# Optimization experiments

Measured on AMD Instinct MI355X. Metric: run time of the kernel, lower is better.

Reference implementation:

```python
import jax, jax.numpy as jnp
import numpy as np
import math

B, L, D, MAXL = 4, 4096, 1024, 16384


def setup_inputs() -> dict:
    key = jax.random.key(0)
    ks = jax.random.split(key, 12)
    s = 0.02
    def w(k, shape):
        return jax.random.normal(k, shape, jnp.float32) * s
    return {
        "x": jax.random.normal(ks[0], (B, L, D), jnp.float32),
        "pos_phases": jax.random.normal(ks[1], (MAXL, D), jnp.float32) * math.pi,
        "Wpv": w(ks[2], (D, D)), "bpv": jnp.zeros((D,), jnp.float32),
        "Wk": w(ks[3], (D, D)), "bk": jnp.zeros((D,), jnp.float32),
        "Wkv": w(ks[4], (D, D)), "bkv": jnp.zeros((D,), jnp.float32),
        "Wg1": w(ks[5], (2 * D, D)), "bg1": jnp.zeros((D,), jnp.float32),
        "Wg2": w(ks[6], (D, 1)), "bg2": jnp.zeros((1,), jnp.float32),
        "Wb1": w(ks[7], (D, D // 2)), "bb1": jnp.zeros((D // 2,), jnp.float32),
        "Wb2": w(ks[8], (D // 2, 2)), "bb2": jnp.zeros((2,), jnp.float32),
        "ln_g": jnp.ones((D,), jnp.float32), "ln_b": jnp.zeros((D,), jnp.float32),
        "Wo": w(ks[9], (D, D)), "bo": jnp.zeros((D,), jnp.float32),
    }


def _shift1(a):
    # torch.roll(a, 1, dims=1) with a[:, 0] = 0
    return jnp.concatenate([jnp.zeros_like(a[:, :1]), a[:, :-1]], axis=1)


def reference(x, pos_phases, Wpv, bpv, Wk, bk, Wkv, bkv, Wg1, bg1, Wg2, bg2,
              Wb1, bb1, Wb2, bb2, ln_g, ln_b, Wo, bo):
    Bq, Lq, Dq = x.shape
    sqrtD = jnp.sqrt(jnp.float32(Dq))

    # positional phasor memory
    pp = pos_phases[:Lq]                      # [L, D]
    pos_cos, pos_sin = jnp.cos(pp), jnp.sin(pp)
    pos_values = x @ Wpv + bpv                # [B, L, D]
    pos_mem_cos = jnp.cumsum(pos_cos * pos_values, axis=1)
    pos_mem_sin = jnp.cumsum(pos_sin * pos_values, axis=1)
    pos_ret = (pos_cos * pos_mem_cos + pos_sin * pos_mem_sin) / sqrtD

    # key-value phasor memory
    key_ph = jnp.tanh(x @ Wk + bk) * jnp.pi
    key_cos, key_sin = jnp.cos(key_ph), jnp.sin(key_ph)
    kv_values = x @ Wkv + bkv

    x_shifted = _shift1(x)
    gate_in = jnp.concatenate([x, x_shifted], axis=-1)       # [B, L, 2D]
    gh = jax.nn.gelu(gate_in @ Wg1 + bg1, approximate=False)
    value_gates = jax.nn.sigmoid(gh @ Wg2 + bg2)             # [B, L, 1]

    kc_s = _shift1(key_cos)
    ks_s = _shift1(key_sin)
    kv_mem_cos = jnp.cumsum(kc_s * kv_values * value_gates, axis=1)
    kv_mem_sin = jnp.cumsum(ks_s * kv_values * value_gates, axis=1)
    gate_cumsum = jnp.maximum(jnp.cumsum(value_gates, axis=1), 1.0)
    kv_ret = (key_cos * kv_mem_cos + key_sin * kv_mem_sin) / (jnp.sqrt(gate_cumsum) * sqrtD)

    # blend
    bh = jax.nn.gelu(x @ Wb1 + bb1, approximate=False)
    bw = jax.nn.softmax(bh @ Wb2 + bb2, axis=-1)             # [B, L, 2]
    blended = bw[..., 0:1] * pos_ret + bw[..., 1:2] * kv_ret

    # to_out: LayerNorm then Linear
    mu = jnp.mean(blended, axis=-1, keepdims=True)
    var = jnp.var(blended, axis=-1, keepdims=True)
    ln = (blended - mu) / jnp.sqrt(var + 1e-5) * ln_g + ln_b
    return x + ln @ Wo + bo
```

## Files before the change

### kernel.cpp

```cpp
#include <hip/hip_runtime.h>
#include <hip/hip_bf16.h>
#include <math.h>

using bf16 = __hip_bfloat16;
typedef __bf16 v8bf __attribute__((ext_vector_type(8)));
typedef float v4f __attribute__((ext_vector_type(4)));

#define B_ 4
#define L_ 4096
#define D_ 1024
#define M_ (B_*L_)
#define CCH 128
#define LCH (L_/CCH)
#define NF 3584

__device__ __forceinline__ float bf2f(bf16 v){ return __bfloat162float(v); }
__device__ __forceinline__ bf16 f2bf(float v){ return __float2bfloat16(v); }
__device__ __forceinline__ float us2f(ushort u){ union{unsigned u32; float f;}c; c.u32=((unsigned)u)<<16; return c.f; }
__device__ __forceinline__ ushort f2us(float v){ bf16 h=__float2bfloat16(v); return *(ushort*)&h; }
__device__ __forceinline__ float h2f(ushort u){ union{ushort s; _Float16 h;}c; c.s=u; return (float)c.h; }
__device__ __forceinline__ ushort f2h(float v){ union{ushort s; _Float16 h;}c; c.h=(_Float16)v; return c.s; }

__device__ __forceinline__ void g2l16(const void* g, void* l){
  __builtin_amdgcn_global_load_lds(
    (const __attribute__((address_space(1))) unsigned int*)g,
    (__attribute__((address_space(3))) unsigned int*)l, 16, 0, 0);
}

__global__ void k_zeroN(float* __restrict__ p, int n){
  int i = blockIdx.x*256 + threadIdx.x;
  if (i < n) p[i] = 0.0f;
}

__global__ void k_cvt(const float* __restrict__ in, bf16* __restrict__ out){
  int i = (blockIdx.x*256 + threadIdx.x)*4;
  float4 v = *(const float4*)(in + i);
  out[i]   = f2bf(v.x);
  out[i+1] = f2bf(v.y);
  out[i+2] = f2bf(v.z);
  out[i+3] = f2bf(v.w);
}

__global__ void k_cvt_pp(const float* __restrict__ in, ushort* __restrict__ out){
  int i = (blockIdx.x*256 + threadIdx.x)*4;
  float4 v = *(const float4*)(in + i);
  out[i]   = f2h(v.x);
  out[i+1] = f2h(v.y);
  out[i+2] = f2h(v.z);
  out[i+3] = f2h(v.w);
}

__global__ void k_ctr(const float* __restrict__ in, bf16* __restrict__ out, int R, int C){
  __shared__ float tile[32][33];
  int c0 = blockIdx.x*32, r0 = blockIdx.y*32;
  #pragma unroll
  for (int i=0;i<32;i+=8)
    tile[threadIdx.y+i][threadIdx.x] = in[(size_t)(r0+threadIdx.y+i)*C + c0+threadIdx.x];
  __syncthreads();
  #pragma unroll
  for (int i=0;i<32;i+=8)
    out[(size_t)(c0+threadIdx.y+i)*R + r0+threadIdx.x] = f2bf(tile[threadIdx.x][threadIdx.y+i]);
}

__global__ void k_pack_bias(const float* __restrict__ bpv, const float* __restrict__ bk,
                            const float* __restrict__ bkv, const float* __restrict__ bb1,
                            float* __restrict__ bf){
  int i = blockIdx.x*256 + threadIdx.x;
  float v;
  if (i < 1024) v = bpv[i];
  else if (i < 2048) v = bk[i-1024];
  else if (i < 3072) v = bkv[i-2048];
  else v = bb1[i-3072];
  bf[i] = v;
}

__device__ __forceinline__ float geluf(float v){
  return 0.5f*v*(1.0f + erff(v*0.70710678118654752f));
}
__device__ __forceinline__ float fast_tanh(float v){
  float a = fabsf(v);
  float e = __expf(-2.0f*a);
  float t = (1.0f - e)/(1.0f + e);
  return copysignf(t, v);
}

#define BM 256
#define BN 256
#define BK 64

template<int EPI, bool CONCAT>
__global__ __launch_bounds__(512) void k_gemm(
    const bf16* __restrict__ A, int lda,
    const bf16* __restrict__ Bt, int ldb,
    const float* __restrict__ bias,
    const bf16* __restrict__ zeros,
    bf16* __restrict__ o_pv, ushort* __restrict__ o_kp, bf16* __restrict__ o_kv,
    const float* __restrict__ Wv2, const float* __restrict__ Wb2f,
    float* __restrict__ gaccp, float* __restrict__ bwaccp,
    float* __restrict__ outf, const float* __restrict__ residf,
    int N, int Ktot)
{
  __shared__ __align__(16) ushort As[2*BM*BK];
  __shared__ __align__(16) ushort Bs[2*BN*BK];
  int tid = threadIdx.x;
  int lane = tid & 63, wave = tid >> 6;
  int wm = wave >> 2, wn = wave & 3;
  int bn = blockIdx.x * BN, bm = blockIdx.y * BM;

  v4f zero = {0.f,0.f,0.f,0.f};
  v4f acc[8][4];
  #pragma unroll
  for (int i=0;i<8;i++)
    #pragma unroll
    for (int j=0;j<4;j++) acc[i][j] = zero;

  int mr = lane & 15, g4 = lane >> 4;
  int srow = lane >> 3, sseg = lane & 7;

  auto stage = [&](int t, int buf){
    int kk = t*BK;
    ushort* Ad = As + buf*(BM*BK);
    ushort* Bd = Bs + buf*(BN*BK);
    #pragma unroll
    for (int p=0;p<4;p++){
      int r = p*64 + wave*8 + srow;
      const bf16* src;
      if (!CONCAT || kk < D_) {
        src = A + (size_t)(bm + r)*lda + (size_t)kk + sseg*8;
      } else {
        int m = bm + r;
        int l = m & (L_-1);
        src = (l==0) ? (zeros + sseg*8)
                     : (A + (size_t)(m-1)*lda + (size_t)(kk - D_) + sseg*8);
      }
      g2l16(src, Ad + (size_t)(p*64 + wave*8)*BK);
    }
    #pragma unroll
    for (int p=0;p<4;p++){
      int r = p*64 + wave*8 + srow;
      g2l16(Bt + (size_t)(bn + r)*ldb + (size_t)kk + sseg*8,
            Bd + (size_t)(p*64 + wave*8)*BK);
    }
  };

  auto compute = [&](int buf){
    const ushort* Ab = As + buf*(BM*BK);
    const ushort* Bb = Bs + buf*(BN*BK);
    #pragma unroll
    for (int ks=0; ks<2; ks++){
      v8bf a[8], b[4];
      #pragma unroll
      for (int i=0;i<8;i++) a[i] = *(const v8bf*)&Ab[(wm*128 + i*16 + mr)*BK + ks*32 + g4*8];
      #pragma unroll
      for (int j=0;j<4;j++) b[j] = *(const v8bf*)&Bb[(wn*64  + j*16 + mr)*BK + ks*32 + g4*8];
      #pragma unroll
      for (int i=0;i<8;i++)
        #pragma unroll
        for (int j=0;j<4;j++)
          acc[i][j] = __builtin_amdgcn_mfma_f32_16x16x32_bf16(a[i], b[j], acc[i][j], 0, 0, 0);
    }
  };

  int nt = Ktot / BK;
  stage(0, 0);
  for (int t=0; t<nt; ++t){
    if (t+1 < nt){
      stage(t+1, (t+1)&1);
      asm volatile("s_waitcnt vmcnt(8)" ::: "memory");
    } else {
      asm volatile("s_waitcnt vmcnt(0)" ::: "memory");
    }
    asm volatile("s_barrier" ::: "memory");
    compute(t&1);
    asm volatile("s_waitcnt lgkmcnt(0)" ::: "memory");
    asm volatile("s_barrier" ::: "memory");
  }

  int lr = lane >> 4, lc = lane & 15;
  if (EPI == 3){
    #pragma unroll
    for (int i=0;i<8;i++){
      #pragma unroll
      for (int j=0;j<4;j++){
        int col  = bn + wn*64 + j*16 + lc;
        int row0 = bm + wm*128 + i*16 + lr*4;
        float bias_v = bias[col];
        #pragma unroll
        for (int rr=0; rr<4; rr++){
          size_t idx = (size_t)(row0+rr)*N + col;
          outf[idx] = acc[i][j][rr] + bias_v + residf[idx];
        }
      }
    }
  } else if (EPI == 2){
    #pragma unroll
    for (int i=0;i<8;i++){
      float red[4] = {0.f,0.f,0.f,0.f};
      #pragma unroll
      for (int j=0;j<4;j++){
        int col = bn + wn*64 + j*16 + lc;
        float bias_v = bias[col];
        float wv = Wv2[col];
        #pragma unroll
        for (int rr=0; rr<4; rr++){
          float v = acc[i][j][rr] + bias_v;
          red[rr] += geluf(v) * wv;
        }
      }
      int row0 = bm + wm*128 + i*16 + lr*4;
      #pragma unroll
      for (int rr=0; rr<4; rr++){
        float r = red[rr];
        r += __shfl_xor(r,1); r += __shfl_xor(r,2);
        r += __shfl_xor(r,4); r += __shfl_xor(r,8);
        if (lc == 0) atomicAdd(&gaccp[row0+rr], r);
      }
    }
  } else {
    if (bn < 3072){
      #pragma unroll
      for (int i=0;i<8;i++){
        #pragma unroll
        for (int j=0;j<4;j++){
          int col  = bn + wn*64 + j*16 + lc;
          int row0 = bm + wm*128 + i*16 + lr*4;
          float bias_v = bias[col];
          #pragma unroll
          for (int rr=0; rr<4; rr++){
            int row = row0 + rr;
            float v = acc[i][j][rr] + bias_v;
            if (bn < 1024) {
              o_pv[(size_t)row*1024 + col] = f2bf(v);
            } else if (bn < 2048) {
              float kp = fast_tanh(v) * 3.14159265358979323846f;
              o_kp[(size_t)row*1024 + (col-1024)] = f2h(kp);
            } else {
              o_kv[(size_t)row*1024 + (col-2048)] = f2bf(v);
            }
          }
        }
      }
    } else {
      #pragma unroll
      for (int i=0;i<8;i++){
        float r0[4] = {0.f,0.f,0.f,0.f};
        float r1[4] = {0.f,0.f,0.f,0.f};
        #pragma unroll
        for (int j=0;j<4;j++){
          int col = bn + wn*64 + j*16 + lc;
          float bias_v = bias[col];
          int kb = col - 3072;
          float w0 = Wb2f[kb*2], w1 = Wb2f[kb*2+1];
          #pragma unroll
          for (int rr=0; rr<4; rr++){
            float v = acc[i][j][rr] + bias_v;
            float gl = geluf(v);
            r0[rr] += gl*w0;
            r1[rr] += gl*w1;
          }
        }
        int row0 = bm + wm*128 + i*16 + lr*4;
        #pragma unroll
        for (int rr=0; rr<4; rr++){
          float a = r0[rr], b = r1[rr];
          a += __shfl_xor(a,1); a += __shfl_xor(a,2); a += __shfl_xor(a,4); a += __shfl_xor(a,8);
          b += __shfl_xor(b,1); b += __shfl_xor(b,2); b += __shfl_xor(b,4); b += __shfl_xor(b,8);
          if (lc == 0){
            atomicAdd(&bwaccp[(size_t)(row0+rr)*2],   a);
            atomicAdd(&bwaccp[(size_t)(row0+rr)*2+1], b);
          }
        }
      }
    }
  }
}

__global__ __launch_bounds__(1024) void k_gscan(const float* __restrict__ gacc,
                                                const float* __restrict__ bg2,
                                                float* __restrict__ g, float* __restrict__ gc){
  __shared__ float sa[1024];
  int b = blockIdx.x, tid = threadIdx.x;
  int base = b*L_ + tid*4;
  float bb = bg2[0];
  float v0 = 1.f/(1.f+__expf(-(gacc[base]   + bb)));
  float v1 = 1.f/(1.f+__expf(-(gacc[base+1] + bb)));
  float v2 = 1.f/(1.f+__expf(-(gacc[base+2] + bb)));
  float v3 = 1.f/(1.f+__expf(-(gacc[base+3] + bb)));
  float s0 = v0, s1 = s0+v1, s2 = s1+v2, s3 = s2+v3;
  sa[tid] = s3; __syncthreads();
  for (int o=1;o<1024;o<<=1){
    float t = sa[tid] + ((tid>=o) ? sa[tid-o] : 0.f);
    __syncthreads();
    sa[tid] = t;
    __syncthreads();
  }
  float ex = sa[tid] - s3;
  g[base]=v0; g[base+1]=v1; g[base+2]=v2; g[base+3]=v3;
  gc[base]=ex+s0; gc[base+1]=ex+s1; gc[base+2]=ex+s2; gc[base+3]=ex+s3;
}

__global__ void k_finishbw(const float* __restrict__ bwacc, const float* __restrict__ bb2,
                           float2* __restrict__ bw){
  int t = blockIdx.x*256 + threadIdx.x;
  float a = bwacc[(size_t)t*2]   + bb2[0];
  float b = bwacc[(size_t)t*2+1] + bb2[1];
  float m = fmaxf(a,b);
  float e0 = __expf(a-m), e1 = __expf(b-m);
  float inv = 1.0f/(e0+e1);
  bw[t] = make_float2(e0*inv, e1*inv);
}

__global__ void k_scan_partial(const bf16* __restrict__ PV, const bf16* __restrict__ KV,
                               const ushort* __restrict__ KP, const float* __restrict__ g,
                               const ushort* __restrict__ ppH, float* __restrict__ PS){
  int tid = threadIdx.x;
  int d0 = tid*4;
  int j = blockIdx.x, b = blockIdx.y;
  int l0 = j*LCH;
  float pkc[4]={0,0,0,0}, pks[4]={0,0,0,0};
  if (l0 > 0){
    size_t pidx = ((size_t)b*L_ + l0-1)*D_ + d0;
    ushort4 up = *(const ushort4*)(KP+pidx);
    float ph0=h2f(up.x), ph1=h2f(up.y), ph2=h2f(up.z), ph3=h2f(up.w);
    __sincosf(ph0,&pks[0],&pkc[0]); __sincosf(ph1,&pks[1],&pkc[1]);
    __sincosf(ph2,&pks[2],&pkc[2]); __sincosf(ph3,&pks[3],&pkc[3]);
  }
  float p0[4]={0,0,0,0}, p1[4]={0,0,0,0}, p2[4]={0,0,0,0}, p3[4]={0,0,0,0};
  for (int l=l0; l<l0+LCH; l++){
    size_t idx = ((size_t)b*L_ + l)*D_ + d0;
    ushort4 upv = *(const ushort4*)(PV+idx);
    ushort4 ukv = *(const ushort4*)(KV+idx);
    ushort4 ukp = *(const ushort4*)(KP+idx);
    ushort4 upp = *(const ushort4*)(ppH + (size_t)l*D_ + d0);
    float gl = g[b*L_ + l];
    float pvv[4]={us2f(upv.x),us2f(upv.y),us2f(upv.z),us2f(upv.w)};
    float kvv[4]={us2f(ukv.x),us2f(ukv.y),us2f(ukv.z),us2f(ukv.w)};
    float kpv[4]={h2f(ukp.x),h2f(ukp.y),h2f(ukp.z),h2f(ukp.w)};
    float phv[4]={h2f(upp.x),h2f(upp.y),h2f(upp.z),h2f(upp.w)};
    #pragma unroll
    for (int c=0;c<4;c++){
      float sn, cs; __sincosf(phv[c], &sn, &cs);
      float kc, ks; __sincosf(kpv[c], &ks, &kc);
      float kvg = kvv[c]*gl;
      p0[c] += cs*pvv[c]; p1[c] += sn*pvv[c];
      p2[c] += pkc[c]*kvg; p3[c] += pks[c]*kvg;
      pkc[c]=kc; pks[c]=ks;
    }
  }
  size_t base = ((size_t)b*CCH + j)*D_ + d0;
  size_t plane = (size_t)B_*CCH*D_;
  #pragma unroll
  for (int c=0;c<4;c++){
    PS[0*plane + base + c] = p0[c];
    PS[1*plane + base + c] = p1[c];
    PS[2*plane + base + c] = p2[c];
    PS[3*plane + base + c] = p3[c];
  }
}

__global__ void k_prefix(float* __restrict__ PS){
  int idx = blockIdx.x*256 + threadIdx.x;
  int q = idx >> 12;
  int rem = idx & 4095;
  int b = rem >> 10, d = rem & 1023;
  size_t plane = (size_t)B_*CCH*D_;
  float* base = PS + (size_t)q*plane + (size_t)b*CCH*D_ + d;
  float s = 0.0f;
  for (int j=0;j<CCH;j+=4){
    float v0 = base[(size_t)(j  )*D_];
    float v1 = base[(size_t)(j+1)*D_];
    float v2 = base[(size_t)(j+2)*D_];
    float v3 = base[(size_t)(j+3)*D_];
    base[(size_t)(j  )*D_] = s; s += v0;
    base[(size_t)(j+1)*D_] = s; s += v1;
    base[(size_t)(j+2)*D_] = s; s += v2;
    base[(size_t)(j+3)*D_] = s; s += v3;
  }
}

__global__ void k_scan_apply(const bf16* __restrict__ PV, const bf16* __restrict__ KV,
                             const ushort* __restrict__ KP, const float* __restrict__ g,
                             const ushort* __restrict__ ppH, const float* __restrict__ PS,
                             const float* __restrict__ gc, const float2* __restrict__ bw,
                             const float* __restrict__ ln_g, const float* __restrict__ ln_b,
                             bf16* __restrict__ LNB){
  __shared__ float sA[4], sB[4];
  int tid = threadIdx.x;
  int d0 = tid*4;
  int j = blockIdx.x, b = blockIdx.y;
  int l0 = j*LCH;
  size_t base = ((size_t)b*CCH + j)*D_ + d0;
  size_t plane = (size_t)B_*CCH*D_;
  float mc[4], ms[4], kcm[4], ksm[4];
  #pragma unroll
  for (int c=0;c<4;c++){
    mc[c]  = PS[0*plane+base+c]; ms[c]  = PS[1*plane+base+c];
    kcm[c] = PS[2*plane+base+c]; ksm[c] = PS[3*plane+base+c];
  }
  float pkc[4]={0,0,0,0}, pks[4]={0,0,0,0};
  if (l0 > 0){
    size_t pidx = ((size_t)b*L_ + l0-1)*D_ + d0;
    ushort4 up = *(const ushort4*)(KP+pidx);
    float ph0=h2f(up.x), ph1=h2f(up.y), ph2=h2f(up.z), ph3=h2f(up.w);
    __sincosf(ph0,&pks[0],&pkc[0]); __sincosf(ph1,&pks[1],&pkc[1]);
    __sincosf(ph2,&pks[2],&pkc[2]); __sincosf(ph3,&pks[3],&pkc[3]);
  }
  float4 gv = *(const float4*)&ln_g[d0];
  float4 bv = *(const float4*)&ln_b[d0];
  int wv = tid >> 6, ln = tid & 63;
  for (int l=l0; l<l0+LCH; l++){
    size_t idx = ((size_t)b*L_ + l)*D_ + d0;
    ushort4 upv = *(const ushort4*)(PV+idx);
    ushort4 ukv = *(const ushort4*)(KV+idx);
    ushort4 ukp = *(const ushort4*)(KP+idx);
    ushort4 upp = *(const ushort4*)(ppH + (size_t)l*D_ + d0);
    float gl = g[b*L_ + l];
    float gcv = fmaxf(gc[b*L_+l], 1.0f);
    float rs = 0.03125f * rsqrtf(gcv);
    float2 w = bw[b*L_+l];
    float pvv[4]={us2f(upv.x),us2f(upv.y),us2f(upv.z),us2f(upv.w)};
    float kvv[4]={us2f(ukv.x),us2f(ukv.y),us2f(ukv.z),us2f(ukv.w)};
    float kpv[4]={h2f(ukp.x),h2f(ukp.y),h2f(ukp.z),h2f(ukp.w)};
    float phv[4]={h2f(upp.x),h2f(upp.y),h2f(upp.z),h2f(upp.w)};
    float bl[4];
    #pragma unroll
    for (int c=0;c<4;c++){
      float sn, cs; __sincosf(phv[c], &sn, &cs);
      float kc, ks; __sincosf(kpv[c], &ks, &kc);
      mc[c] += cs*pvv[c]; ms[c] += sn*pvv[c];
      float pos_ret = (cs*mc[c] + sn*ms[c]) * 0.03125f;
      float kvg = kvv[c]*gl;
      kcm[c] += pkc[c]*kvg; ksm[c] += pks[c]*kvg;
      float kv_ret = (kc*kcm[c] + ks*ksm[c]) * rs;
      bl[c] = w.x*pos_ret + w.y*kv_ret;
      pkc[c]=kc; pks[c]=ks;
    }
    float s  = bl[0]+bl[1]+bl[2]+bl[3];
    float s2 = bl[0]*bl[0]+bl[1]*bl[1]+bl[2]*bl[2]+bl[3]*bl[3];
    #pragma unroll
    for (int o=1;o<64;o<<=1){ s += __shfl_xor(s,o); s2 += __shfl_xor(s2,o); }
    if (ln == 0){ sA[wv] = s; sB[wv] = s2; }
    __syncthreads();
    float ts  = sA[0]+sA[1]+sA[2]+sA[3];
    float ts2 = sB[0]+sB[1]+sB[2]+sB[3];
    __syncthreads();
    float mu   = ts * (1.0f/D_);
    float var  = ts2 * (1.0f/D_) - mu*mu;
    float rstd = rsqrtf(var + 1e-5f);
    ushort4 ou;
    ou.x = f2us((bl[0]-mu)*rstd*gv.x + bv.x);
    ou.y = f2us((bl[1]-mu)*rstd*gv.y + bv.y);
    ou.z = f2us((bl[2]-mu)*rstd*gv.z + bv.z);
    ou.w = f2us((bl[3]-mu)*rstd*gv.w + bv.w);
    *(ushort4*)((ushort*)LNB + idx) = ou;
  }
}

extern "C" void kernel_launch(void* const* d_in, const int* in_sizes, int n_in,
                              void* d_out, int out_size, void* d_ws, size_t ws_size,
                              hipStream_t stream) {
  const float* x     = (const float*)d_in[0];
  const float* phases= (const float*)d_in[1];
  const float* Wpv   = (const float*)d_in[2];
  const float* bpv   = (const float*)d_in[3];
  const float* Wk    = (const float*)d_in[4];
  const float* bk    = (const float*)d_in[5];
  const float* Wkv   = (const float*)d_in[6];
  const float* bkv   = (const float*)d_in[7];
  const float* Wg1   = (const float*)d_in[8];
  const float* bg1   = (const float*)d_in[9];
  const float* Wg2   = (const float*)d_in[10];
  const float* bg2   = (const float*)d_in[11];
  const float* Wb1   = (const float*)d_in[12];
  const float* bb1   = (const float*)d_in[13];
  const float* Wb2   = (const float*)d_in[14];
  const float* bb2   = (const float*)d_in[15];
  const float* ln_g  = (const float*)d_in[16];
  const float* ln_b  = (const float*)d_in[17];
  const float* Wo    = (const float*)d_in[18];
  const float* bo    = (const float*)d_in[19];
  float* out = (float*)d_out;

  char* ws = (char*)d_ws;
  size_t off = 0;
  auto alloc = [&](size_t bytes)->char*{
    char* p = ws + off; off += (bytes + 255) & ~(size_t)255; return p;
  };
  bf16*  xb   = (bf16*)alloc((size_t)M_*D_*2);
  bf16*  WfT  = (bf16*)alloc((size_t)NF*D_*2);
  bf16*  Wg1T = (bf16*)alloc((size_t)D_*2*D_*2);
  bf16*  WoT  = (bf16*)alloc((size_t)D_*D_*2);
  bf16*  PV   = (bf16*)alloc((size_t)M_*D_*2);
  bf16*  KV   = (bf16*)alloc((size_t)M_*D_*2);
  ushort* KP  = (ushort*)alloc((size_t)M_*D_*2);
  ushort* ppH = (ushort*)alloc((size_t)L_*D_*2);
  bf16*  LNB  = (bf16*)alloc((size_t)M_*D_*2);
  float* gbuf  = (float*)alloc((size_t)M_*4);
  float* gcbuf = (float*)alloc((size_t)M_*4);
  float2* bwbuf= (float2*)alloc((size_t)M_*8);
  float* PS    = (float*)alloc((size_t)4*B_*CCH*D_*4);
  float* biasF = (float*)alloc((size_t)NF*4);
  float* gacc  = (float*)alloc((size_t)M_*4);
  float* bwacc = (float*)alloc((size_t)M_*2*4);
  bf16*  zeros = (bf16*)alloc(256);
  int nzero = (M_ + 2*M_ + 64);

  k_zeroN<<<(nzero+255)/256,256,0,stream>>>(gacc, nzero);
  k_cvt<<<(M_*D_)/1024, 256, 0, stream>>>(x, xb);
  k_cvt_pp<<<(L_*D_)/1024, 256, 0, stream>>>(phases, ppH);

  dim3 tb(32,8);
  k_ctr<<<dim3(D_/32, D_/32), tb, 0, stream>>>(Wpv, WfT,                       D_, D_);
  k_ctr<<<dim3(D_/32, D_/32), tb, 0, stream>>>(Wk,  WfT + (size_t)1024*D_,     D_, D_);
  k_ctr<<<dim3(D_/32, D_/32), tb, 0, stream>>>(Wkv, WfT + (size_t)2048*D_,     D_, D_);
  k_ctr<<<dim3((D_/2)/32, D_/32), tb, 0, stream>>>(Wb1, WfT + (size_t)3072*D_, D_, D_/2);
  k_ctr<<<dim3(D_/32, 2*D_/32), tb, 0, stream>>>(Wg1, Wg1T, 2*D_, D_);
  k_ctr<<<dim3(D_/32, D_/32), tb, 0, stream>>>(Wo,  WoT,  D_, D_);
  k_pack_bias<<<NF/256,256,0,stream>>>(bpv, bk, bkv, bb1, biasF);

  k_gemm<4,false><<<dim3(NF/BN, M_/BM),512,0,stream>>>(
      xb, D_, WfT, D_, biasF, zeros, PV, KP, KV, nullptr, Wb2, nullptr, bwacc,
      nullptr, nullptr, NF, D_);
  k_gemm<2,true><<<dim3(D_/BN, M_/BM),512,0,stream>>>(
      xb, D_, Wg1T, 2*D_, bg1, zeros, nullptr, nullptr, nullptr, Wg2, nullptr, gacc, nullptr,
      nullptr, nullptr, D_, 2*D_);
  k_gscan<<<B_,1024,0,stream>>>(gacc, bg2, gbuf, gcbuf);
  k_finishbw<<<M_/256,256,0,stream>>>(bwacc, bb2, bwbuf);
  dim3 sg(CCH, B_);
  k_scan_partial<<<sg,256,0,stream>>>(PV, KV, KP, gbuf, ppH, PS);
  k_prefix<<<(4*B_*D_)/256,256,0,stream>>>(PS);
  k_scan_apply<<<sg,256,0,stream>>>(PV, KV, KP, gbuf, ppH, PS, gcbuf, bwbuf, ln_g, ln_b, LNB);
  k_gemm<3,false><<<dim3(D_/BN, M_/BM),512,0,stream>>>(
      LNB, D_, WoT, D_, bo, zeros, nullptr, nullptr, nullptr, nullptr, nullptr, nullptr, nullptr,
      out, x, D_, D_);
}
```

Before: 661.1 us.

## Restructure GEMM mainloop into four-quadrant ping-pong with swizzled LDS and setprio

The GEMM main loop now splits each K-tile into four quadrant stages. Loads for the next tile are issued in halves interleaved between MFMA groups, separated by barriers and s_setprio hints, so global-to-LDS traffic overlaps compute. LDS rows use an XOR swizzle on both the global-load source column and the ds_read address to remove bank conflicts. The wave-to-output mapping changes to quadrant form, and the epilogues are reindexed to match. The extra barriers and the tighter waitcnt bookkeeping add synchronisation overhead and risk correctness errors.

```diff
diff --git a/kernel.cpp b/kernel.cpp
--- a/kernel.cpp
+++ b/kernel.cpp
@@ -116,98 +116,159 @@
 
   int mr = lane & 15, g4 = lane >> 4;
   int srow = lane >> 3, sseg = lane & 7;
-
-  auto stage = [&](int t, int buf){
-    int kk = t*BK;
-    ushort* Ad = As + buf*(BM*BK);
-    ushort* Bd = Bs + buf*(BN*BK);
-    #pragma unroll
-    for (int p=0;p<4;p++){
-      int r = p*64 + wave*8 + srow;
+  int swzs = (sseg ^ srow) * 8;
+
+  auto stage_half = [&](int t, int which){
+    int buf = t & 1;
+    int kk = t * BK;
+    bool isA = (which==0) || (which==3);
+    int rbase = (which==0 || which==1) ? 0 : 128;
+    ushort* dst = (isA ? As : Bs) + buf*(BM*BK);
+    #pragma unroll
+    for (int p=0;p<2;p++){
+      int r = rbase + p*64 + wave*8 + srow;
       const bf16* src;
-      if (!CONCAT || kk < D_) {
-        src = A + (size_t)(bm + r)*lda + (size_t)kk + sseg*8;
+      if (isA){
+        if (!CONCAT || kk < D_) {
+          src = A + (size_t)(bm + r)*lda + (size_t)kk + swzs;
+        } else {
+          int m = bm + r;
+          int l = m & (L_-1);
+          src = (l==0) ? (zeros + swzs)
+                       : (A + (size_t)(m-1)*lda + (size_t)(kk - D_) + swzs);
+        }
       } else {
-        int m = bm + r;
-        int l = m & (L_-1);
-        src = (l==0) ? (zeros + sseg*8)
-                     : (A + (size_t)(m-1)*lda + (size_t)(kk - D_) + sseg*8);
-      }
-      g2l16(src, Ad + (size_t)(p*64 + wave*8)*BK);
-    }
-    #pragma unroll
-    for (int p=0;p<4;p++){
-      int r = p*64 + wave*8 + srow;
-      g2l16(Bt + (size_t)(bn + r)*ldb + (size_t)kk + sseg*8,
-            Bd + (size_t)(p*64 + wave*8)*BK);
+        src = Bt + (size_t)(bn + r)*ldb + (size_t)kk + swzs;
+      }
+      g2l16(src, dst + (size_t)(rbase + p*64 + wave*8)*BK);
     }
   };
 
-  auto compute = [&](int buf){
-    const ushort* Ab = As + buf*(BM*BK);
-    const ushort* Bb = Bs + buf*(BN*BK);
-    #pragma unroll
-    for (int ks=0; ks<2; ks++){
-      v8bf a[8], b[4];
-      #pragma unroll
-      for (int i=0;i<8;i++) a[i] = *(const v8bf*)&Ab[(wm*128 + i*16 + mr)*BK + ks*32 + g4*8];
-      #pragma unroll
-      for (int j=0;j<4;j++) b[j] = *(const v8bf*)&Bb[(wn*64  + j*16 + mr)*BK + ks*32 + g4*8];
-      #pragma unroll
-      for (int i=0;i<8;i++)
-        #pragma unroll
-        for (int j=0;j<4;j++)
-          acc[i][j] = __builtin_amdgcn_mfma_f32_16x16x32_bf16(a[i], b[j], acc[i][j], 0, 0, 0);
-    }
+  auto lds_a = [&](const ushort* Ab, int ih, int i, int ks)->v8bf{
+    int row = ih*128 + wm*64 + i*16 + mr;
+    int off = row*128 + ((ks*64 + g4*16) ^ ((mr&7)<<4));
+    return *(const v8bf*)((const char*)Ab + off);
   };
+  auto lds_b = [&](const ushort* Bb, int jh, int j, int ks)->v8bf{
+    int row = jh*128 + wn*32 + j*16 + mr;
+    int off = row*128 + ((ks*64 + g4*16) ^ ((mr&7)<<4));
+    return *(const v8bf*)((const char*)Bb + off);
+  };
 
   int nt = Ktot / BK;
-  stage(0, 0);
+  stage_half(0,0); stage_half(0,1); stage_half(0,2); stage_half(0,3);
+  asm volatile("s_waitcnt vmcnt(4)" ::: "memory");
+  asm volatile("s_barrier" ::: "memory");
+
+  v8bf a[4][2];
+  v8bf b[2][2][2];
+
   for (int t=0; t<nt; ++t){
-    if (t+1 < nt){
-      stage(t+1, (t+1)&1);
-      asm volatile("s_waitcnt vmcnt(8)" ::: "memory");
-    } else {
-      asm volatile("s_waitcnt vmcnt(0)" ::: "memory");
-    }
-    asm volatile("s_barrier" ::: "memory");
-    compute(t&1);
+    const ushort* Ab = As + (t&1)*(BM*BK);
+    const ushort* Bb = Bs + (t&1)*(BM*BK);
+    bool more = (t+1 < nt);
+
+    #pragma unroll
+    for (int i=0;i<4;i++){ a[i][0] = lds_a(Ab,0,i,0); a[i][1] = lds_a(Ab,0,i,1); }
+    #pragma unroll
+    for (int j=0;j<2;j++){ b[0][j][0] = lds_b(Bb,0,j,0); b[0][j][1] = lds_b(Bb,0,j,1); }
+    if (more) stage_half(t+1, 0);
+    asm volatile("s_barrier" ::: "memory");
     asm volatile("s_waitcnt lgkmcnt(0)" ::: "memory");
+    __builtin_amdgcn_s_setprio(1);
+    #pragma unroll
+    for (int i=0;i<4;i++)
+      #pragma unroll
+      for (int j=0;j<2;j++){
+        acc[i][j] = __builtin_amdgcn_mfma_f32_16x16x32_bf16(a[i][0], b[0][j][0], acc[i][j], 0,0,0);
+        acc[i][j] = __builtin_amdgcn_mfma_f32_16x16x32_bf16(a[i][1], b[0][j][1], acc[i][j], 0,0,0);
+      }
+    __builtin_amdgcn_s_setprio(0);
+    if (more) asm volatile("s_waitcnt vmcnt(4)" ::: "memory");
+    else      asm volatile("s_waitcnt vmcnt(2)" ::: "memory");
+    asm volatile("s_barrier" ::: "memory");
+
+    #pragma unroll
+    for (int j=0;j<2;j++){ b[1][j][0] = lds_b(Bb,1,j,0); b[1][j][1] = lds_b(Bb,1,j,1); }
+    if (more) stage_half(t+1, 1);
+    asm volatile("s_barrier" ::: "memory");
+    asm volatile("s_waitcnt lgkmcnt(0)" ::: "memory");
+    __builtin_amdgcn_s_setprio(1);
+    #pragma unroll
+    for (int i=0;i<4;i++)
+      #pragma unroll
+      for (int j=0;j<2;j++){
+        acc[i][2+j] = __builtin_amdgcn_mfma_f32_16x16x32_bf16(a[i][0], b[1][j][0], acc[i][2+j], 0,0,0);
+        acc[i][2+j] = __builtin_amdgcn_mfma_f32_16x16x32_bf16(a[i][1], b[1][j][1], acc[i][2+j], 0,0,0);
+      }
+    __builtin_amdgcn_s_setprio(0);
+    if (more) asm volatile("s_waitcnt vmcnt(4)" ::: "memory");
+    else      asm volatile("s_waitcnt vmcnt(0)" ::: "memory");
+    asm volatile("s_barrier" ::: "memory");
+
+    #pragma unroll
+    for (int i=0;i<4;i++){ a[i][0] = lds_a(Ab,1,i,0); a[i][1] = lds_a(Ab,1,i,1); }
+    if (more) stage_half(t+1, 2);
+    asm volatile("s_barrier" ::: "memory");
+    asm volatile("s_waitcnt lgkmcnt(0)" ::: "memory");
+    __builtin_amdgcn_s_setprio(1);
+    #pragma unroll
+    for (int i=0;i<4;i++)
+      #pragma unroll
+      for (int j=0;j<2;j++){
+        acc[4+i][2+j] = __builtin_amdgcn_mfma_f32_16x16x32_bf16(a[i][0], b[1][j][0], acc[4+i][2+j], 0,0,0);
+        acc[4+i][2+j] = __builtin_amdgcn_mfma_f32_16x16x32_bf16(a[i][1], b[1][j][1], acc[4+i][2+j], 0,0,0);
+      }
+    __builtin_amdgcn_s_setprio(0);
+    asm volatile("s_barrier" ::: "memory");
+
+    if (more) stage_half(t+1, 3);
+    asm volatile("s_barrier" ::: "memory");
+    __builtin_amdgcn_s_setprio(1);
+    #pragma unroll
+    for (int i=0;i<4;i++)
+      #pragma unroll
+      for (int j=0;j<2;j++){
+        acc[4+i][j] = __builtin_amdgcn_mfma_f32_16x16x32_bf16(a[i][0], b[0][j][0], acc[4+i][j], 0,0,0);
+        acc[4+i][j] = __builtin_amdgcn_mfma_f32_16x16x32_bf16(a[i][1], b[0][j][1], acc[4+i][j], 0,0,0);
+      }
+    __builtin_amdgcn_s_setprio(0);
+    if (more) asm volatile("s_waitcnt vmcnt(4)" ::: "memory");
     asm volatile("s_barrier" ::: "memory");
   }
 
   int lr = lane >> 4, lc = lane & 15;
   if (EPI == 3){
     #pragma unroll
-    for (int i=0;i<8;i++){
-      #pragma unroll
-      for (int j=0;j<4;j++){
-        int col  = bn + wn*64 + j*16 + lc;
-        int row0 = bm + wm*128 + i*16 + lr*4;
+    for (int ai=0;ai<8;ai++){
+      #pragma unroll
+      for (int bj=0;bj<4;bj++){
+        int col  = bn + (bj>>1)*128 + wn*32 + (bj&1)*16 + lc;
+        int row0 = bm + (ai>>2)*128 + wm*64 + (ai&3)*16 + lr*4;
         float bias_v = bias[col];
         #pragma unroll
         for (int rr=0; rr<4; rr++){
           size_t idx = (size_t)(row0+rr)*N + col;
-          outf[idx] = acc[i][j][rr] + bias_v + residf[idx];
+          outf[idx] = acc[ai][bj][rr] + bias_v + residf[idx];
         }
       }
     }
   } else if (EPI == 2){
     #pragma unroll
-    for (int i=0;i<8;i++){
+    for (int ai=0;ai<8;ai++){
       float red[4] = {0.f,0.f,0.f,0.f};
       #pragma unroll
-      for (int j=0;j<4;j++){
-        int col = bn + wn*64 + j*16 + lc;
+      for (int bj=0;bj<4;bj++){
+        int col = bn + (bj>>1)*128 + wn*32 + (bj&1)*16 + lc;
         float bias_v = bias[col];
         float wv = Wv2[col];
         #pragma unroll
         for (int rr=0; rr<4; rr++){
-          float v = acc[i][j][rr] + bias_v;
+          float v = acc[ai][bj][rr] + bias_v;
           red[rr] += geluf(v) * wv;
         }
       }
-      int row0 = bm + wm*128 + i*16 + lr*4;
+      int row0 = bm + (ai>>2)*128 + wm*64 + (ai&3)*16 + lr*4;
       #pragma unroll
       for (int rr=0; rr<4; rr++){
         float r = red[rr];
@@ -219,16 +280,16 @@
   } else {
     if (bn < 3072){
       #pragma unroll
-      for (int i=0;i<8;i++){
+      for (int ai=0;ai<8;ai++){
         #pragma unroll
-        for (int j=0;j<4;j++){
-          int col  = bn + wn*64 + j*16 + lc;
-          int row0 = bm + wm*128 + i*16 + lr*4;
+        for (int bj=0;bj<4;bj++){
+          int col  = bn + (bj>>1)*128 + wn*32 + (bj&1)*16 + lc;
+          int row0 = bm + (ai>>2)*128 + wm*64 + (ai&3)*16 + lr*4;
           float bias_v = bias[col];
           #pragma unroll
           for (int rr=0; rr<4; rr++){
             int row = row0 + rr;
-            float v = acc[i][j][rr] + bias_v;
+            float v = acc[ai][bj][rr] + bias_v;
             if (bn < 1024) {
               o_pv[(size_t)row*1024 + col] = f2bf(v);
             } else if (bn < 2048) {
@@ -242,32 +303,32 @@
       }
     } else {
       #pragma unroll
-      for (int i=0;i<8;i++){
+      for (int ai=0;ai<8;ai++){
         float r0[4] = {0.f,0.f,0.f,0.f};
         float r1[4] = {0.f,0.f,0.f,0.f};
         #pragma unroll
-        for (int j=0;j<4;j++){
-          int col = bn + wn*64 + j*16 + lc;
+        for (int bj=0;bj<4;bj++){
+          int col = bn + (bj>>1)*128 + wn*32 + (bj&1)*16 + lc;
           float bias_v = bias[col];
           int kb = col - 3072;
           float w0 = Wb2f[kb*2], w1 = Wb2f[kb*2+1];
           #pragma unroll
           for (int rr=0; rr<4; rr++){
-            float v = acc[i][j][rr] + bias_v;
+            float v = acc[ai][bj][rr] + bias_v;
             float gl = geluf(v);
             r0[rr] += gl*w0;
             r1[rr] += gl*w1;
           }
         }
-        int row0 = bm + wm*128 + i*16 + lr*4;
+        int row0 = bm + (ai>>2)*128 + wm*64 + (ai&3)*16 + lr*4;
         #pragma unroll
         for (int rr=0; rr<4; rr++){
-          float a = r0[rr], b = r1[rr];
-          a += __shfl_xor(a,1); a += __shfl_xor(a,2); a += __shfl_xor(a,4); a += __shfl_xor(a,8);
-          b += __shfl_xor(b,1); b += __shfl_xor(b,2); b += __shfl_xor(b,4); b += __shfl_xor(b,8);
+          float a2 = r0[rr], b2 = r1[rr];
+          a2 += __shfl_xor(a2,1); a2 += __shfl_xor(a2,2); a2 += __shfl_xor(a2,4); a2 += __shfl_xor(a2,8);
+          b2 += __shfl_xor(b2,1); b2 += __shfl_xor(b2,2); b2 += __shfl_xor(b2,4); b2 += __shfl_xor(b2,8);
           if (lc == 0){
-            atomicAdd(&bwaccp[(size_t)(row0+rr)*2],   a);
-            atomicAdd(&bwaccp[(size_t)(row0+rr)*2+1], b);
+            atomicAdd(&bwaccp[(size_t)(row0+rr)*2],   a2);
+            atomicAdd(&bwaccp[(size_t)(row0+rr)*2+1], b2);
           }
         }
       }
```

After: 599.3 us. 1.1x faster.
